# Performance work log

Measured on AMD Instinct MI355X. Metric: run time of the kernel, lower is better.

## Reference

```python
import jax, jax.numpy as jnp
import numpy as np

D_MODEL = 512
NUM_HEADS = 8
D_K = D_MODEL // NUM_HEADS
SCALE = D_K ** (-0.5)
B, L = 2, 256


def _tropical_linear(x, W, b):
    # max-plus linear: y[..., o] = max_i (x[..., i] + W[o, i]) + b[o]
    # x: (B, L, Din), W: (Dout, Din)
    return jnp.max(x[:, :, None, :] + W[None, None, :, :], axis=-1) + b


def _split_heads(t):
    Bn, Ln, Dn = t.shape
    return t.reshape(Bn, Ln, NUM_HEADS, D_K).transpose(0, 2, 1, 3)  # (B,H,L,dk)


def setup_inputs() -> dict:
    key = jax.random.key(0)
    ks = jax.random.split(key, 8)
    s = 1.0 / np.sqrt(D_MODEL)
    return {
        "x": jax.random.normal(ks[0], (B, L, D_MODEL), jnp.float32),
        "qW": jax.random.normal(ks[1], (D_MODEL, D_MODEL), jnp.float32) * s,
        "qb": jnp.zeros((D_MODEL,), jnp.float32),
        "kW": jax.random.normal(ks[2], (D_MODEL, D_MODEL), jnp.float32) * s,
        "kb": jnp.zeros((D_MODEL,), jnp.float32),
        "vW": jax.random.normal(ks[3], (D_MODEL, D_MODEL), jnp.float32) * s,
        "vb": jnp.zeros((D_MODEL,), jnp.float32),
        "oW": jax.random.normal(ks[4], (D_MODEL, D_MODEL), jnp.float32) * s,
        "ob": jnp.zeros((D_MODEL,), jnp.float32),
        "gW": jnp.zeros((NUM_HEADS, D_MODEL), jnp.float32),  # torch init: zeros
        "gb": jnp.full((NUM_HEADS,), 2.0, jnp.float32),      # torch init: +2.0
        "temp": jnp.ones((NUM_HEADS,), jnp.float32),
    }


def reference(x, qW, qb, kW, kb, vW, vb, oW, ob, gW, gb, temp):
    Bn, Ln, Dn = x.shape
    Q = _split_heads(_tropical_linear(x, qW, qb))  # (B,H,L,dk)
    K = _split_heads(_tropical_linear(x, kW, kb))
    V = _split_heads(x @ vW.T + vb)

    class_scores = jnp.einsum('bhqd,bhkd->bhqk', Q, K) * SCALE
    # tropical max-plus scores: max_d (Q[q,d] + K[k,d])
    trop_scores = jnp.max(Q[:, :, :, None, :] + K[:, :, None, :, :], axis=-1) * SCALE

    g = jax.nn.sigmoid(x @ gW.T + gb)            # (B,L,H)
    g = g.transpose(0, 2, 1)[..., None]          # (B,H,L,1)
    scores = g * trop_scores + (1.0 - g) * class_scores

    # Maslov temperature softmax: per-head learnable temperature
    attn = jax.nn.softmax(scores / temp[None, :, None, None], axis=-1)

    out = jnp.einsum('bhqk,bhkd->bhqd', attn, V)
    out = out.transpose(0, 2, 1, 3).reshape(Bn, Ln, Dn)
    return out @ oW.T + ob, attn
```

## Files before the change

kernel.cpp:

```cpp
#include <hip/hip_runtime.h>
#include <math.h>

#define DM    512
#define LSEQ  256
#define NB    2
#define NH    8
#define DK    64
#define SCALEF 0.125f

__global__ __launch_bounds__(256) void qkvg_kernel(
    const float* __restrict__ x,
    const float* __restrict__ qW, const float* __restrict__ qb,
    const float* __restrict__ kW, const float* __restrict__ kb,
    const float* __restrict__ vW, const float* __restrict__ vb,
    const float* __restrict__ gW, const float* __restrict__ gb,
    float* __restrict__ Qo, float* __restrict__ Ko,
    float* __restrict__ Vo, float* __restrict__ go)
{
    const int tid = threadIdx.x;
    const int op  = blockIdx.z;

    if (op == 3) {
        if (blockIdx.y != 0) return;
        const int row = blockIdx.x * 32 + (tid >> 3);
        const int h   = tid & 7;
        const float4* xr = (const float4*)(x  + row * DM);
        const float4* wr = (const float4*)(gW + h  * DM);
        float acc = 0.f;
        #pragma unroll 8
        for (int i = 0; i < DM / 4; ++i) {
            float4 a = xr[i], w = wr[i];
            acc = fmaf(a.x, w.x, acc);
            acc = fmaf(a.y, w.y, acc);
            acc = fmaf(a.z, w.z, acc);
            acc = fmaf(a.w, w.w, acc);
        }
        acc += gb[h];
        go[row * NH + h] = 1.f / (1.f + __expf(-acc));
        return;
    }

    const float* __restrict__ W;
    const float* __restrict__ bias;
    float* __restrict__ out;
    bool trop;
    if      (op == 0) { W = qW; bias = qb; out = Qo; trop = true;  }
    else if (op == 1) { W = kW; bias = kb; out = Ko; trop = true;  }
    else              { W = vW; bias = vb; out = Vo; trop = false; }

    __shared__ float Xs[32][68];
    __shared__ float Ws[32][68];

    const int row0 = blockIdx.x * 32;
    const int col0 = blockIdx.y * 32;
    const int ty = tid >> 4, tx = tid & 15;
    const int ra = ty;
    const int c4 = tx * 4;

    const float* xp0 = x + (row0 + ra) * DM + c4;
    const float* xp1 = xp0 + 16 * DM;
    const float* wp0 = W + (col0 + ra) * DM + c4;
    const float* wp1 = wp0 + 16 * DM;

    float4 xv0 = *(const float4*)xp0;
    float4 xv1 = *(const float4*)xp1;
    float4 wv0 = *(const float4*)wp0;
    float4 wv1 = *(const float4*)wp1;

    const float init = trop ? -INFINITY : 0.f;
    float a00 = init, a01 = init, a10 = init, a11 = init;

    for (int k0 = 0; k0 < DM; k0 += 64) {
        __syncthreads();
        *(float4*)&Xs[ra     ][c4] = xv0;
        *(float4*)&Xs[ra + 16][c4] = xv1;
        *(float4*)&Ws[ra     ][c4] = wv0;
        *(float4*)&Ws[ra + 16][c4] = wv1;
        __syncthreads();
        if (k0 + 64 < DM) {
            xv0 = *(const float4*)(xp0 + k0 + 64);
            xv1 = *(const float4*)(xp1 + k0 + 64);
            wv0 = *(const float4*)(wp0 + k0 + 64);
            wv1 = *(const float4*)(wp1 + k0 + 64);
        }
        if (trop) {
            #pragma unroll
            for (int kq = 0; kq < 16; ++kq) {
                float4 x0 = *(const float4*)&Xs[ty*2    ][kq*4];
                float4 x1 = *(const float4*)&Xs[ty*2 + 1][kq*4];
                float4 w0 = *(const float4*)&Ws[tx*2    ][kq*4];
                float4 w1 = *(const float4*)&Ws[tx*2 + 1][kq*4];
                a00 = fmaxf(fmaxf(a00, x0.x + w0.x), x0.y + w0.y);
                a00 = fmaxf(fmaxf(a00, x0.z + w0.z), x0.w + w0.w);
                a01 = fmaxf(fmaxf(a01, x0.x + w1.x), x0.y + w1.y);
                a01 = fmaxf(fmaxf(a01, x0.z + w1.z), x0.w + w1.w);
                a10 = fmaxf(fmaxf(a10, x1.x + w0.x), x1.y + w0.y);
                a10 = fmaxf(fmaxf(a10, x1.z + w0.z), x1.w + w0.w);
                a11 = fmaxf(fmaxf(a11, x1.x + w1.x), x1.y + w1.y);
                a11 = fmaxf(fmaxf(a11, x1.z + w1.z), x1.w + w1.w);
            }
        } else {
            #pragma unroll
            for (int kq = 0; kq < 16; ++kq) {
                float4 x0 = *(const float4*)&Xs[ty*2    ][kq*4];
                float4 x1 = *(const float4*)&Xs[ty*2 + 1][kq*4];
                float4 w0 = *(const float4*)&Ws[tx*2    ][kq*4];
                float4 w1 = *(const float4*)&Ws[tx*2 + 1][kq*4];
                a00 = fmaf(x0.x, w0.x, a00); a00 = fmaf(x0.y, w0.y, a00);
                a00 = fmaf(x0.z, w0.z, a00); a00 = fmaf(x0.w, w0.w, a00);
                a01 = fmaf(x0.x, w1.x, a01); a01 = fmaf(x0.y, w1.y, a01);
                a01 = fmaf(x0.z, w1.z, a01); a01 = fmaf(x0.w, w1.w, a01);
                a10 = fmaf(x1.x, w0.x, a10); a10 = fmaf(x1.y, w0.y, a10);
                a10 = fmaf(x1.z, w0.z, a10); a10 = fmaf(x1.w, w0.w, a10);
                a11 = fmaf(x1.x, w1.x, a11); a11 = fmaf(x1.y, w1.y, a11);
                a11 = fmaf(x1.z, w1.z, a11); a11 = fmaf(x1.w, w1.w, a11);
            }
        }
    }

    const int r0 = row0 + ty * 2, c0 = col0 + tx * 2;
    const float b0 = bias[c0], b1 = bias[c0 + 1];
    *(float2*)&out[(size_t)r0      * DM + c0] = make_float2(a00 + b0, a01 + b1);
    *(float2*)&out[(size_t)(r0+1)  * DM + c0] = make_float2(a10 + b0, a11 + b1);
}

__global__ __launch_bounds__(512) void attn_kernel(
    const float* __restrict__ Q, const float* __restrict__ K,
    const float* __restrict__ V, const float* __restrict__ g,
    const float* __restrict__ temp,
    float* __restrict__ attn_out, float* __restrict__ hout)
{
    const int tid = threadIdx.x;
    const int bh  = blockIdx.y;
    const int b   = bh >> 3, h = bh & 7;
    const int q0  = blockIdx.x * 16;
    const int ty  = tid >> 5;
    const int tx  = tid & 31;

    __shared__ float Qs[16][68];
    __shared__ float KVs[64][68];
    __shared__ float Ss[16][260];

    if (tid < 256) {
        const int r = tid >> 4, c = (tid & 15) * 4;
        float4 v = *(const float4*)&Q[(b * LSEQ + q0 + r) * DM + h * DK + c];
        *(float4*)&Qs[r][c] = v;
    }
    const float gq   = g[(b * LSEQ + q0 + ty) * NH + h];
    const float invt = SCALEF / temp[h];

    for (int kt = 0; kt < 4; ++kt) {
        __syncthreads();
        #pragma unroll
        for (int i = 0; i < 2; ++i) {
            const int f = tid + 512 * i;
            const int r = f >> 4, c = (f & 15) * 4;
            float4 v = *(const float4*)&K[(b * LSEQ + kt * 64 + r) * DM + h * DK + c];
            *(float4*)&KVs[r][c] = v;
        }
        __syncthreads();
        float d0 = 0.f, d1 = 0.f;
        float t0 = -INFINITY, t1 = -INFINITY;
        #pragma unroll
        for (int dq = 0; dq < 16; ++dq) {
            float4 q  = *(const float4*)&Qs[ty][dq * 4];
            float4 k0 = *(const float4*)&KVs[tx     ][dq * 4];
            float4 k1 = *(const float4*)&KVs[tx + 32][dq * 4];
            d0 = fmaf(q.x, k0.x, d0); d0 = fmaf(q.y, k0.y, d0);
            d0 = fmaf(q.z, k0.z, d0); d0 = fmaf(q.w, k0.w, d0);
            d1 = fmaf(q.x, k1.x, d1); d1 = fmaf(q.y, k1.y, d1);
            d1 = fmaf(q.z, k1.z, d1); d1 = fmaf(q.w, k1.w, d1);
            t0 = fmaxf(fmaxf(t0, q.x + k0.x), q.y + k0.y);
            t0 = fmaxf(fmaxf(t0, q.z + k0.z), q.w + k0.w);
            t1 = fmaxf(fmaxf(t1, q.x + k1.x), q.y + k1.y);
            t1 = fmaxf(fmaxf(t1, q.z + k1.z), q.w + k1.w);
        }
        Ss[ty][kt*64 + tx     ] = (gq * t0 + (1.f - gq) * d0) * invt;
        Ss[ty][kt*64 + tx + 32] = (gq * t1 + (1.f - gq) * d1) * invt;
    }
    __syncthreads();

    {
        float m = -INFINITY;
        #pragma unroll
        for (int j = 0; j < 8; ++j) m = fmaxf(m, Ss[ty][tx + 32 * j]);
        #pragma unroll
        for (int o = 16; o; o >>= 1) m = fmaxf(m, __shfl_xor(m, o));
        float s = 0.f;
        #pragma unroll
        for (int j = 0; j < 8; ++j) {
            const float e = __expf(Ss[ty][tx + 32 * j] - m);
            Ss[ty][tx + 32 * j] = e;
            s += e;
        }
        #pragma unroll
        for (int o = 16; o; o >>= 1) s += __shfl_xor(s, o);
        const float rs = 1.f / s;
        #pragma unroll
        for (int j = 0; j < 8; ++j) Ss[ty][tx + 32 * j] *= rs;
    }
    __syncthreads();

    {
        float* dst = attn_out + (size_t)(bh * LSEQ + q0) * LSEQ;
        #pragma unroll
        for (int i = 0; i < 2; ++i) {
            const int fi  = i * 2048 + tid * 4;
            const int row = fi >> 8, col = fi & 255;
            float4 v = *(const float4*)&Ss[row][col];
            *(float4*)&dst[fi] = v;
        }
    }

    float acc0 = 0.f, acc1 = 0.f;
    for (int kt = 0; kt < 4; ++kt) {
        __syncthreads();
        #pragma unroll
        for (int i = 0; i < 2; ++i) {
            const int f = tid + 512 * i;
            const int r = f >> 4, c = (f & 15) * 4;
            float4 v = *(const float4*)&V[(b * LSEQ + kt * 64 + r) * DM + h * DK + c];
            *(float4*)&KVs[r][c] = v;
        }
        __syncthreads();
        #pragma unroll
        for (int kq = 0; kq < 16; ++kq) {
            float4 a = *(const float4*)&Ss[ty][kt * 64 + kq * 4];
            const int k = kq * 4;
            float2 v0 = *(const float2*)&KVs[k    ][tx * 2];
            float2 v1 = *(const float2*)&KVs[k + 1][tx * 2];
            float2 v2 = *(const float2*)&KVs[k + 2][tx * 2];
            float2 v3 = *(const float2*)&KVs[k + 3][tx * 2];
            acc0 = fmaf(a.x, v0.x, acc0); acc1 = fmaf(a.x, v0.y, acc1);
            acc0 = fmaf(a.y, v1.x, acc0); acc1 = fmaf(a.y, v1.y, acc1);
            acc0 = fmaf(a.z, v2.x, acc0); acc1 = fmaf(a.z, v2.y, acc1);
            acc0 = fmaf(a.w, v3.x, acc0); acc1 = fmaf(a.w, v3.y, acc1);
        }
    }
    *(float2*)&hout[(size_t)(bh * LSEQ + q0 + ty) * DK + tx * 2] =
        make_float2(acc0, acc1);
}

__global__ __launch_bounds__(256) void oproj_kernel(
    const float* __restrict__ hout,
    const float* __restrict__ oW, const float* __restrict__ ob,
    float* __restrict__ out)
{
    __shared__ float Xs[32][68];
    __shared__ float Ws[32][68];
    const int tid = threadIdx.x;
    const int ty = tid >> 4, tx = tid & 15;
    const int row0 = blockIdx.x * 32;
    const int col0 = blockIdx.y * 32;
    const int ra = ty;
    const int c4 = tx * 4;

    const int grow = row0 + ra;
    const int bb = grow >> 8, ll = grow & 255;

    const float* wp0 = oW + (col0 + ra) * DM + c4;
    const float* wp1 = wp0 + 16 * DM;

    float a00 = 0.f, a01 = 0.f, a10 = 0.f, a11 = 0.f;

    float4 xv0 = *(const float4*)&hout[((bb * NH + 0) * LSEQ + ll     ) * DK + c4];
    float4 xv1 = *(const float4*)&hout[((bb * NH + 0) * LSEQ + ll + 16) * DK + c4];
    float4 wv0 = *(const float4*)wp0;
    float4 wv1 = *(const float4*)wp1;

    for (int k0 = 0; k0 < DM; k0 += 64) {
        __syncthreads();
        *(float4*)&Xs[ra     ][c4] = xv0;
        *(float4*)&Xs[ra + 16][c4] = xv1;
        *(float4*)&Ws[ra     ][c4] = wv0;
        *(float4*)&Ws[ra + 16][c4] = wv1;
        __syncthreads();
        if (k0 + 64 < DM) {
            const int hh = (k0 >> 6) + 1;
            xv0 = *(const float4*)&hout[((bb * NH + hh) * LSEQ + ll     ) * DK + c4];
            xv1 = *(const float4*)&hout[((bb * NH + hh) * LSEQ + ll + 16) * DK + c4];
            wv0 = *(const float4*)(wp0 + k0 + 64);
            wv1 = *(const float4*)(wp1 + k0 + 64);
        }
        #pragma unroll
        for (int kq = 0; kq < 16; ++kq) {
            float4 x0 = *(const float4*)&Xs[ty*2    ][kq*4];
            float4 x1 = *(const float4*)&Xs[ty*2 + 1][kq*4];
            float4 w0 = *(const float4*)&Ws[tx*2    ][kq*4];
            float4 w1 = *(const float4*)&Ws[tx*2 + 1][kq*4];
            a00 = fmaf(x0.x, w0.x, a00); a00 = fmaf(x0.y, w0.y, a00);
            a00 = fmaf(x0.z, w0.z, a00); a00 = fmaf(x0.w, w0.w, a00);
            a01 = fmaf(x0.x, w1.x, a01); a01 = fmaf(x0.y, w1.y, a01);
            a01 = fmaf(x0.z, w1.z, a01); a01 = fmaf(x0.w, w1.w, a01);
            a10 = fmaf(x1.x, w0.x, a10); a10 = fmaf(x1.y, w0.y, a10);
            a10 = fmaf(x1.z, w0.z, a10); a10 = fmaf(x1.w, w0.w, a10);
            a11 = fmaf(x1.x, w1.x, a11); a11 = fmaf(x1.y, w1.y, a11);
            a11 = fmaf(x1.z, w1.z, a11); a11 = fmaf(x1.w, w1.w, a11);
        }
    }

    const int r0 = row0 + ty * 2, c0 = col0 + tx * 2;
    const float b0 = ob[c0], b1 = ob[c0 + 1];
    *(float2*)&out[(size_t)r0     * DM + c0] = make_float2(a00 + b0, a01 + b1);
    *(float2*)&out[(size_t)(r0+1) * DM + c0] = make_float2(a10 + b0, a11 + b1);
}

extern "C" void kernel_launch(void* const* d_in, const int* in_sizes, int n_in,
                              void* d_out, int out_size, void* d_ws, size_t ws_size,
                              hipStream_t stream)
{
    const float* x    = (const float*)d_in[0];
    const float* qW   = (const float*)d_in[1];
    const float* qb   = (const float*)d_in[2];
    const float* kW   = (const float*)d_in[3];
    const float* kb   = (const float*)d_in[4];
    const float* vW   = (const float*)d_in[5];
    const float* vb   = (const float*)d_in[6];
    const float* oW   = (const float*)d_in[7];
    const float* ob   = (const float*)d_in[8];
    const float* gW   = (const float*)d_in[9];
    const float* gb   = (const float*)d_in[10];
    const float* temp = (const float*)d_in[11];

    float* out      = (float*)d_out;
    float* attn_out = out + NB * LSEQ * DM;

    float* ws   = (float*)d_ws;
    float* Qo   = ws;
    float* Ko   = Qo + NB * LSEQ * DM;
    float* Vo   = Ko + NB * LSEQ * DM;
    float* go   = Vo + NB * LSEQ * DM;
    float* hout = go + NB * LSEQ * NH;

    qkvg_kernel<<<dim3(16, 16, 4), 256, 0, stream>>>(
        x, qW, qb, kW, kb, vW, vb, gW, gb, Qo, Ko, Vo, go);
    attn_kernel<<<dim3(16, 16), 512, 0, stream>>>(
        Qo, Ko, Vo, go, temp, attn_out, hout);
    oproj_kernel<<<dim3(16, 16), 256, 0, stream>>>(
        hout, oW, ob, out);
}
```

Before: 163.8 us.

## Retile all three kernels with larger register tiles and transposed smem layouts

The QKV projection moves from 32x32 tiles with 2x2 outputs per thread to 64x64 tiles with 4x4 outputs per thread, using a k-major transposed shared layout and a flattened 1D grid of 192 GEMM blocks plus 16 gate blocks. The attention kernel drops to 256 threads, keeps Q in registers, stores K transposed, and computes 4 keys per thread. Head outputs are now written in (B,L,D) layout, so the output projection reads them contiguously using an outer-product 2x2 tile. The aim is more arithmetic per shared-memory load and less redundant traffic, at the cost of fewer blocks (lower occupancy and parallelism) and higher register pressure.

```diff
diff --git a/kernel.cpp b/kernel.cpp
--- a/kernel.cpp
+++ b/kernel.cpp
@@ -7,6 +7,7 @@
 #define NH    8
 #define DK    64
 #define SCALEF 0.125f
+#define KC    64
 
 __global__ __launch_bounds__(256) void qkvg_kernel(
     const float* __restrict__ x,
@@ -18,11 +19,11 @@
     float* __restrict__ Vo, float* __restrict__ go)
 {
     const int tid = threadIdx.x;
-    const int op  = blockIdx.z;
-
-    if (op == 3) {
-        if (blockIdx.y != 0) return;
-        const int row = blockIdx.x * 32 + (tid >> 3);
+    const int bx  = blockIdx.x;
+
+    if (bx >= 192) {
+        const int gx  = bx - 192;
+        const int row = gx * 32 + (tid >> 3);
         const int h   = tid & 7;
         const float4* xr = (const float4*)(x  + row * DM);
         const float4* wr = (const float4*)(gW + h  * DM);
@@ -40,6 +41,12 @@
         return;
     }
 
+    const int rt = bx / 24;
+    const int ct = bx % 24;
+    const int op = ct >> 3;
+    const int row0  = rt * 64;
+    const int col0m = (ct & 7) * 64;
+
     const float* __restrict__ W;
     const float* __restrict__ bias;
     float* __restrict__ out;
@@ -48,83 +55,101 @@
     else if (op == 1) { W = kW; bias = kb; out = Ko; trop = true;  }
     else              { W = vW; bias = vb; out = Vo; trop = false; }
 
-    __shared__ float Xs[32][68];
-    __shared__ float Ws[32][68];
-
-    const int row0 = blockIdx.x * 32;
-    const int col0 = blockIdx.y * 32;
+    __shared__ float Xs[KC][68];
+    __shared__ float Ws[KC][68];
+
     const int ty = tid >> 4, tx = tid & 15;
-    const int ra = ty;
-    const int c4 = tx * 4;
-
-    const float* xp0 = x + (row0 + ra) * DM + c4;
-    const float* xp1 = xp0 + 16 * DM;
-    const float* wp0 = W + (col0 + ra) * DM + c4;
-    const float* wp1 = wp0 + 16 * DM;
-
-    float4 xv0 = *(const float4*)xp0;
-    float4 xv1 = *(const float4*)xp1;
-    float4 wv0 = *(const float4*)wp0;
-    float4 wv1 = *(const float4*)wp1;
+    const int sr = tid & 63;
+    const int sq = tid >> 6;
+
+    const float* xp = x + (row0  + sr) * DM + sq * 16;
+    const float* wp = W + (col0m + sr) * DM + sq * 16;
+
+    float4 xg[4], wg[4];
+    #pragma unroll
+    for (int i = 0; i < 4; ++i) {
+        xg[i] = *(const float4*)(xp + i * 4);
+        wg[i] = *(const float4*)(wp + i * 4);
+    }
 
     const float init = trop ? -INFINITY : 0.f;
-    float a00 = init, a01 = init, a10 = init, a11 = init;
-
-    for (int k0 = 0; k0 < DM; k0 += 64) {
-        __syncthreads();
-        *(float4*)&Xs[ra     ][c4] = xv0;
-        *(float4*)&Xs[ra + 16][c4] = xv1;
-        *(float4*)&Ws[ra     ][c4] = wv0;
-        *(float4*)&Ws[ra + 16][c4] = wv1;
-        __syncthreads();
-        if (k0 + 64 < DM) {
-            xv0 = *(const float4*)(xp0 + k0 + 64);
-            xv1 = *(const float4*)(xp1 + k0 + 64);
-            wv0 = *(const float4*)(wp0 + k0 + 64);
-            wv1 = *(const float4*)(wp1 + k0 + 64);
+    float acc[4][4];
+    #pragma unroll
+    for (int i = 0; i < 4; ++i)
+        #pragma unroll
+        for (int j = 0; j < 4; ++j) acc[i][j] = init;
+
+    for (int k0 = 0; k0 < DM; k0 += KC) {
+        __syncthreads();
+        #pragma unroll
+        for (int i = 0; i < 4; ++i) {
+            const int kk = sq * 16 + i * 4;
+            Xs[kk + 0][sr] = xg[i].x;  Xs[kk + 1][sr] = xg[i].y;
+            Xs[kk + 2][sr] = xg[i].z;  Xs[kk + 3][sr] = xg[i].w;
+            Ws[kk + 0][sr] = wg[i].x;  Ws[kk + 1][sr] = wg[i].y;
+            Ws[kk + 2][sr] = wg[i].z;  Ws[kk + 3][sr] = wg[i].w;
+        }
+        __syncthreads();
+        if (k0 + KC < DM) {
+            #pragma unroll
+            for (int i = 0; i < 4; ++i) {
+                xg[i] = *(const float4*)(xp + k0 + KC + i * 4);
+                wg[i] = *(const float4*)(wp + k0 + KC + i * 4);
+            }
         }
         if (trop) {
-            #pragma unroll
-            for (int kq = 0; kq < 16; ++kq) {
-                float4 x0 = *(const float4*)&Xs[ty*2    ][kq*4];
-                float4 x1 = *(const float4*)&Xs[ty*2 + 1][kq*4];
-                float4 w0 = *(const float4*)&Ws[tx*2    ][kq*4];
-                float4 w1 = *(const float4*)&Ws[tx*2 + 1][kq*4];
-                a00 = fmaxf(fmaxf(a00, x0.x + w0.x), x0.y + w0.y);
-                a00 = fmaxf(fmaxf(a00, x0.z + w0.z), x0.w + w0.w);
-                a01 = fmaxf(fmaxf(a01, x0.x + w1.x), x0.y + w1.y);
-                a01 = fmaxf(fmaxf(a01, x0.z + w1.z), x0.w + w1.w);
-                a10 = fmaxf(fmaxf(a10, x1.x + w0.x), x1.y + w0.y);
-                a10 = fmaxf(fmaxf(a10, x1.z + w0.z), x1.w + w0.w);
-                a11 = fmaxf(fmaxf(a11, x1.x + w1.x), x1.y + w1.y);
-                a11 = fmaxf(fmaxf(a11, x1.z + w1.z), x1.w + w1.w);
+            #pragma unroll 4
+            for (int kp = 0; kp < KC / 2; ++kp) {
+                const int kk = kp * 2;
+                float4 x0 = *(const float4*)&Xs[kk    ][ty * 4];
+                float4 x1 = *(const float4*)&Xs[kk + 1][ty * 4];
+                float4 w0 = *(const float4*)&Ws[kk    ][tx * 4];
+                float4 w1 = *(const float4*)&Ws[kk + 1][tx * 4];
+                const float xa0[4] = {x0.x, x0.y, x0.z, x0.w};
+                const float xa1[4] = {x1.x, x1.y, x1.z, x1.w};
+                const float wa0[4] = {w0.x, w0.y, w0.z, w0.w};
+                const float wa1[4] = {w1.x, w1.y, w1.z, w1.w};
+                #pragma unroll
+                for (int i = 0; i < 4; ++i)
+                    #pragma unroll
+                    for (int j = 0; j < 4; ++j)
+                        acc[i][j] = fmaxf(fmaxf(acc[i][j], xa0[i] + wa0[j]),
+                                          xa1[i] + wa1[j]);
             }
         } else {
-            #pragma unroll
-            for (int kq = 0; kq < 16; ++kq) {
-                float4 x0 = *(const float4*)&Xs[ty*2    ][kq*4];
-                float4 x1 = *(const float4*)&Xs[ty*2 + 1][kq*4];
-                float4 w0 = *(const float4*)&Ws[tx*2    ][kq*4];
-                float4 w1 = *(const float4*)&Ws[tx*2 + 1][kq*4];
-                a00 = fmaf(x0.x, w0.x, a00); a00 = fmaf(x0.y, w0.y, a00);
-                a00 = fmaf(x0.z, w0.z, a00); a00 = fmaf(x0.w, w0.w, a00);
-                a01 = fmaf(x0.x, w1.x, a01); a01 = fmaf(x0.y, w1.y, a01);
-                a01 = fmaf(x0.z, w1.z, a01); a01 = fmaf(x0.w, w1.w, a01);
-                a10 = fmaf(x1.x, w0.x, a10); a10 = fmaf(x1.y, w0.y, a10);
-                a10 = fmaf(x1.z, w0.z, a10); a10 = fmaf(x1.w, w0.w, a10);
-                a11 = fmaf(x1.x, w1.x, a11); a11 = fmaf(x1.y, w1.y, a11);
-                a11 = fmaf(x1.z, w1.z, a11); a11 = fmaf(x1.w, w1.w, a11);
-            }
-        }
-    }
-
-    const int r0 = row0 + ty * 2, c0 = col0 + tx * 2;
-    const float b0 = bias[c0], b1 = bias[c0 + 1];
-    *(float2*)&out[(size_t)r0      * DM + c0] = make_float2(a00 + b0, a01 + b1);
-    *(float2*)&out[(size_t)(r0+1)  * DM + c0] = make_float2(a10 + b0, a11 + b1);
+            #pragma unroll 4
+            for (int kp = 0; kp < KC / 2; ++kp) {
+                const int kk = kp * 2;
+                float4 x0 = *(const float4*)&Xs[kk    ][ty * 4];
+                float4 x1 = *(const float4*)&Xs[kk + 1][ty * 4];
+                float4 w0 = *(const float4*)&Ws[kk    ][tx * 4];
+                float4 w1 = *(const float4*)&Ws[kk + 1][tx * 4];
+                const float xa0[4] = {x0.x, x0.y, x0.z, x0.w};
+                const float xa1[4] = {x1.x, x1.y, x1.z, x1.w};
+                const float wa0[4] = {w0.x, w0.y, w0.z, w0.w};
+                const float wa1[4] = {w1.x, w1.y, w1.z, w1.w};
+                #pragma unroll
+                for (int i = 0; i < 4; ++i)
+                    #pragma unroll
+                    for (int j = 0; j < 4; ++j) {
+                        acc[i][j] = fmaf(xa0[i], wa0[j], acc[i][j]);
+                        acc[i][j] = fmaf(xa1[i], wa1[j], acc[i][j]);
+                    }
+            }
+        }
+    }
+
+    const float4 bv = *(const float4*)&bias[col0m + tx * 4];
+    #pragma unroll
+    for (int i = 0; i < 4; ++i) {
+        const int r = row0 + ty * 4 + i;
+        float4 o = make_float4(acc[i][0] + bv.x, acc[i][1] + bv.y,
+                               acc[i][2] + bv.z, acc[i][3] + bv.w);
+        *(float4*)&out[(size_t)r * DM + col0m + tx * 4] = o;
+    }
 }
 
-__global__ __launch_bounds__(512) void attn_kernel(
+__global__ __launch_bounds__(256) void attn_kernel(
     const float* __restrict__ Q, const float* __restrict__ K,
     const float* __restrict__ V, const float* __restrict__ g,
     const float* __restrict__ temp,
@@ -134,111 +159,124 @@
     const int bh  = blockIdx.y;
     const int b   = bh >> 3, h = bh & 7;
     const int q0  = blockIdx.x * 16;
-    const int ty  = tid >> 5;
-    const int tx  = tid & 31;
-
-    __shared__ float Qs[16][68];
-    __shared__ float KVs[64][68];
+    const int ty  = tid >> 4, tx = tid & 15;
+
+    __shared__ float Kd[64][68];
+    __shared__ float Vs[64][68];
     __shared__ float Ss[16][260];
 
-    if (tid < 256) {
-        const int r = tid >> 4, c = (tid & 15) * 4;
-        float4 v = *(const float4*)&Q[(b * LSEQ + q0 + r) * DM + h * DK + c];
-        *(float4*)&Qs[r][c] = v;
-    }
+    const float* qrow = Q + (size_t)(b * LSEQ + q0 + ty) * DM + h * DK;
+    float4 qreg[16];
+    #pragma unroll
+    for (int i = 0; i < 16; ++i) qreg[i] = *(const float4*)(qrow + i * 4);
+
     const float gq   = g[(b * LSEQ + q0 + ty) * NH + h];
     const float invt = SCALEF / temp[h];
 
+    const int sr = tid & 63;
+    const int sq = tid >> 6;
+
     for (int kt = 0; kt < 4; ++kt) {
         __syncthreads();
-        #pragma unroll
-        for (int i = 0; i < 2; ++i) {
-            const int f = tid + 512 * i;
-            const int r = f >> 4, c = (f & 15) * 4;
-            float4 v = *(const float4*)&K[(b * LSEQ + kt * 64 + r) * DM + h * DK + c];
-            *(float4*)&KVs[r][c] = v;
-        }
-        __syncthreads();
-        float d0 = 0.f, d1 = 0.f;
-        float t0 = -INFINITY, t1 = -INFINITY;
-        #pragma unroll
-        for (int dq = 0; dq < 16; ++dq) {
-            float4 q  = *(const float4*)&Qs[ty][dq * 4];
-            float4 k0 = *(const float4*)&KVs[tx     ][dq * 4];
-            float4 k1 = *(const float4*)&KVs[tx + 32][dq * 4];
-            d0 = fmaf(q.x, k0.x, d0); d0 = fmaf(q.y, k0.y, d0);
-            d0 = fmaf(q.z, k0.z, d0); d0 = fmaf(q.w, k0.w, d0);
-            d1 = fmaf(q.x, k1.x, d1); d1 = fmaf(q.y, k1.y, d1);
-            d1 = fmaf(q.z, k1.z, d1); d1 = fmaf(q.w, k1.w, d1);
-            t0 = fmaxf(fmaxf(t0, q.x + k0.x), q.y + k0.y);
-            t0 = fmaxf(fmaxf(t0, q.z + k0.z), q.w + k0.w);
-            t1 = fmaxf(fmaxf(t1, q.x + k1.x), q.y + k1.y);
-            t1 = fmaxf(fmaxf(t1, q.z + k1.z), q.w + k1.w);
-        }
-        Ss[ty][kt*64 + tx     ] = (gq * t0 + (1.f - gq) * d0) * invt;
-        Ss[ty][kt*64 + tx + 32] = (gq * t1 + (1.f - gq) * d1) * invt;
+        {
+            const float* kp = K + (size_t)(b * LSEQ + kt * 64 + sr) * DM
+                              + h * DK + sq * 16;
+            #pragma unroll
+            for (int i = 0; i < 4; ++i) {
+                float4 v = *(const float4*)(kp + i * 4);
+                const int d = sq * 16 + i * 4;
+                Kd[d + 0][sr] = v.x;  Kd[d + 1][sr] = v.y;
+                Kd[d + 2][sr] = v.z;  Kd[d + 3][sr] = v.w;
+            }
+        }
+        __syncthreads();
+        float d0 = 0.f, d1 = 0.f, d2 = 0.f, d3 = 0.f;
+        float t0 = -INFINITY, t1 = -INFINITY, t2 = -INFINITY, t3 = -INFINITY;
+        #pragma unroll
+        for (int k4 = 0; k4 < 16; ++k4) {
+            const float4 q4 = qreg[k4];
+            float4 ka = *(const float4*)&Kd[k4 * 4 + 0][tx * 4];
+            float4 kb = *(const float4*)&Kd[k4 * 4 + 1][tx * 4];
+            float4 kc = *(const float4*)&Kd[k4 * 4 + 2][tx * 4];
+            float4 kd = *(const float4*)&Kd[k4 * 4 + 3][tx * 4];
+            d0 = fmaf(q4.x, ka.x, d0); d0 = fmaf(q4.y, kb.x, d0);
+            d0 = fmaf(q4.z, kc.x, d0); d0 = fmaf(q4.w, kd.x, d0);
+            d1 = fmaf(q4.x, ka.y, d1); d1 = fmaf(q4.y, kb.y, d1);
+            d1 = fmaf(q4.z, kc.y, d1); d1 = fmaf(q4.w, kd.y, d1);
+            d2 = fmaf(q4.x, ka.z, d2); d2 = fmaf(q4.y, kb.z, d2);
+            d2 = fmaf(q4.z, kc.z, d2); d2 = fmaf(q4.w, kd.z, d2);
+            d3 = fmaf(q4.x, ka.w, d3); d3 = fmaf(q4.y, kb.w, d3);
+            d3 = fmaf(q4.z, kc.w, d3); d3 = fmaf(q4.w, kd.w, d3);
+            t0 = fmaxf(fmaxf(t0, q4.x + ka.x), q4.y + kb.x);
+            t0 = fmaxf(fmaxf(t0, q4.z + kc.x), q4.w + kd.x);
+            t1 = fmaxf(fmaxf(t1, q4.x + ka.y), q4.y + kb.y);
+            t1 = fmaxf(fmaxf(t1, q4.z + kc.y), q4.w + kd.y);
+            t2 = fmaxf(fmaxf(t2, q4.x + ka.z), q4.y + kb.z);
+            t2 = fmaxf(fmaxf(t2, q4.z + kc.z), q4.w + kd.z);
+            t3 = fmaxf(fmaxf(t3, q4.x + ka.w), q4.y + kb.w);
+            t3 = fmaxf(fmaxf(t3, q4.z + kc.w), q4.w + kd.w);
+        }
+        const float gi = 1.f - gq;
+        *(float4*)&Ss[ty][kt * 64 + tx * 4] = make_float4(
+            (gq * t0 + gi * d0) * invt, (gq * t1 + gi * d1) * invt,
+            (gq * t2 + gi * d2) * invt, (gq * t3 + gi * d3) * invt);
     }
     __syncthreads();
 
     {
         float m = -INFINITY;
-        #pragma unroll
-        for (int j = 0; j < 8; ++j) m = fmaxf(m, Ss[ty][tx + 32 * j]);
-        #pragma unroll
-        for (int o = 16; o; o >>= 1) m = fmaxf(m, __shfl_xor(m, o));
+        #pragma unroll 4
+        for (int j = 0; j < 16; ++j) m = fmaxf(m, Ss[ty][tx + 16 * j]);
+        #pragma unroll
+        for (int o = 8; o; o >>= 1) m = fmaxf(m, __shfl_xor(m, o));
         float s = 0.f;
-        #pragma unroll
-        for (int j = 0; j < 8; ++j) {
-            const float e = __expf(Ss[ty][tx + 32 * j] - m);
-            Ss[ty][tx + 32 * j] = e;
+        #pragma unroll 4
+        for (int j = 0; j < 16; ++j) {
+            const float e = __expf(Ss[ty][tx + 16 * j] - m);
+            Ss[ty][tx + 16 * j] = e;
             s += e;
         }
         #pragma unroll
-        for (int o = 16; o; o >>= 1) s += __shfl_xor(s, o);
+        for (int o = 8; o; o >>= 1) s += __shfl_xor(s, o);
         const float rs = 1.f / s;
-        #pragma unroll
-        for (int j = 0; j < 8; ++j) Ss[ty][tx + 32 * j] *= rs;
-    }
-    __syncthreads();
+        #pragma unroll 4
+        for (int j = 0; j < 16; ++j) Ss[ty][tx + 16 * j] *= rs;
+    }
 
     {
-        float* dst = attn_out + (size_t)(bh * LSEQ + q0) * LSEQ;
-        #pragma unroll
-        for (int i = 0; i < 2; ++i) {
-            const int fi  = i * 2048 + tid * 4;
-            const int row = fi >> 8, col = fi & 255;
-            float4 v = *(const float4*)&Ss[row][col];
-            *(float4*)&dst[fi] = v;
-        }
-    }
-
-    float acc0 = 0.f, acc1 = 0.f;
+        float* dst = attn_out + (size_t)(bh * LSEQ + q0 + ty) * LSEQ;
+        #pragma unroll
+        for (int j = 0; j < 4; ++j)
+            *(float4*)&dst[j * 64 + tx * 4] =
+                *(const float4*)&Ss[ty][j * 64 + tx * 4];
+    }
+
+    float o0 = 0.f, o1 = 0.f, o2 = 0.f, o3 = 0.f;
+    const int vr = tid & 63;
+    const int vc = tid >> 6;
     for (int kt = 0; kt < 4; ++kt) {
         __syncthreads();
-        #pragma unroll
-        for (int i = 0; i < 2; ++i) {
-            const int f = tid + 512 * i;
-            const int r = f >> 4, c = (f & 15) * 4;
-            float4 v = *(const float4*)&V[(b * LSEQ + kt * 64 + r) * DM + h * DK + c];
-            *(float4*)&KVs[r][c] = v;
-        }
-        __syncthreads();
-        #pragma unroll
-        for (int kq = 0; kq < 16; ++kq) {
-            float4 a = *(const float4*)&Ss[ty][kt * 64 + kq * 4];
-            const int k = kq * 4;
-            float2 v0 = *(const float2*)&KVs[k    ][tx * 2];
-            float2 v1 = *(const float2*)&KVs[k + 1][tx * 2];
-            float2 v2 = *(const float2*)&KVs[k + 2][tx * 2];
-            float2 v3 = *(const float2*)&KVs[k + 3][tx * 2];
-            acc0 = fmaf(a.x, v0.x, acc0); acc1 = fmaf(a.x, v0.y, acc1);
-            acc0 = fmaf(a.y, v1.x, acc0); acc1 = fmaf(a.y, v1.y, acc1);
-            acc0 = fmaf(a.z, v2.x, acc0); acc1 = fmaf(a.z, v2.y, acc1);
-            acc0 = fmaf(a.w, v3.x, acc0); acc1 = fmaf(a.w, v3.y, acc1);
-        }
-    }
-    *(float2*)&hout[(size_t)(bh * LSEQ + q0 + ty) * DK + tx * 2] =
-        make_float2(acc0, acc1);
+        {
+            const float* vp = V + (size_t)(b * LSEQ + kt * 64 + vr) * DM
+                              + h * DK + vc * 16;
+            #pragma unroll
+            for (int i = 0; i < 4; ++i)
+                *(float4*)&Vs[vr][vc * 16 + i * 4] = *(const float4*)(vp + i * 4);
+        }
+        __syncthreads();
+        #pragma unroll 8
+        for (int k2 = 0; k2 < 32; ++k2) {
+            float2 a2 = *(const float2*)&Ss[ty][kt * 64 + k2 * 2];
+            float4 v0 = *(const float4*)&Vs[k2 * 2    ][tx * 4];
+            float4 v1 = *(const float4*)&Vs[k2 * 2 + 1][tx * 4];
+            o0 = fmaf(a2.x, v0.x, o0); o0 = fmaf(a2.y, v1.x, o0);
+            o1 = fmaf(a2.x, v0.y, o1); o1 = fmaf(a2.y, v1.y, o1);
+            o2 = fmaf(a2.x, v0.z, o2); o2 = fmaf(a2.y, v1.z, o2);
+            o3 = fmaf(a2.x, v0.w, o3); o3 = fmaf(a2.y, v1.w, o3);
+        }
+    }
+    *(float4*)&hout[(size_t)(b * LSEQ + q0 + ty) * DM + h * DK + tx * 4] =
+        make_float4(o0, o1, o2, o3);
 }
 
 __global__ __launch_bounds__(256) void oproj_kernel(
@@ -246,63 +284,63 @@
     const float* __restrict__ oW, const float* __restrict__ ob,
     float* __restrict__ out)
 {
-    __shared__ float Xs[32][68];
-    __shared__ float Ws[32][68];
     const int tid = threadIdx.x;
+    const int bx  = blockIdx.x;
+    const int row0 = (bx >> 4) * 32;
+    const int col0 = (bx & 15) * 32;
+
+    __shared__ float Xs[KC][36];
+    __shared__ float Ws[KC][36];
+
     const int ty = tid >> 4, tx = tid & 15;
-    const int row0 = blockIdx.x * 32;
-    const int col0 = blockIdx.y * 32;
-    const int ra = ty;
-    const int c4 = tx * 4;
-
-    const int grow = row0 + ra;
-    const int bb = grow >> 8, ll = grow & 255;
-
-    const float* wp0 = oW + (col0 + ra) * DM + c4;
-    const float* wp1 = wp0 + 16 * DM;
+    const int sr = tid & 31;
+    const int sq = tid >> 5;
+
+    const float* xp = hout + (size_t)(row0 + sr) * DM + sq * 8;
+    const float* wp = oW   + (size_t)(col0 + sr) * DM + sq * 8;
+
+    float4 xg[2], wg[2];
+    #pragma unroll
+    for (int i = 0; i < 2; ++i) {
+        xg[i] = *(const float4*)(xp + i * 4);
+        wg[i] = *(const float4*)(wp + i * 4);
+    }
 
     float a00 = 0.f, a01 = 0.f, a10 = 0.f, a11 = 0.f;
 
-    float4 xv0 = *(const float4*)&hout[((bb * NH + 0) * LSEQ + ll     ) * DK + c4];
-    float4 xv1 = *(const float4*)&hout[((bb * NH + 0) * LSEQ + ll + 16) * DK + c4];
-    float4 wv0 = *(const float4*)wp0;
-    float4 wv1 = *(const float4*)wp1;
-
-    for (int k0 = 0; k0 < DM; k0 += 64) {
-        __syncthreads();
-        *(float4*)&Xs[ra     ][c4] = xv0;
-        *(float4*)&Xs[ra + 16][c4] = xv1;
-        *(float4*)&Ws[ra     ][c4] = wv0;
-        *(float4*)&Ws[ra + 16][c4] = wv1;
-        __syncthreads();
-        if (k0 + 64 < DM) {
-            const int hh = (k0 >> 6) + 1;
-            xv0 = *(const float4*)&hout[((bb * NH + hh) * LSEQ + ll     ) * DK + c4];
-            xv1 = *(const float4*)&hout[((bb * NH + hh) * LSEQ + ll + 16) * DK + c4];
-            wv0 = *(const float4*)(wp0 + k0 + 64);
-            wv1 = *(const float4*)(wp1 + k0 + 64);
-        }
-        #pragma unroll
-        for (int kq = 0; kq < 16; ++kq) {
-            float4 x0 = *(const float4*)&Xs[ty*2    ][kq*4];
-            float4 x1 = *(const float4*)&Xs[ty*2 + 1][kq*4];
-            float4 w0 = *(const float4*)&Ws[tx*2    ][kq*4];
-            float4 w1 = *(const float4*)&Ws[tx*2 + 1][kq*4];
-            a00 = fmaf(x0.x, w0.x, a00); a00 = fmaf(x0.y, w0.y, a00);
-            a00 = fmaf(x0.z, w0.z, a00); a00 = fmaf(x0.w, w0.w, a00);
-            a01 = fmaf(x0.x, w1.x, a01); a01 = fmaf(x0.y, w1.y, a01);
-            a01 = fmaf(x0.z, w1.z, a01); a01 = fmaf(x0.w, w1.w, a01);
-            a10 = fmaf(x1.x, w0.x, a10); a10 = fmaf(x1.y, w0.y, a10);
-            a10 = fmaf(x1.z, w0.z, a10); a10 = fmaf(x1.w, w0.w, a10);
-            a11 = fmaf(x1.x, w1.x, a11); a11 = fmaf(x1.y, w1.y, a11);
-            a11 = fmaf(x1.z, w1.z, a11); a11 = fmaf(x1.w, w1.w, a11);
+    for (int k0 = 0; k0 < DM; k0 += KC) {
+        __syncthreads();
+        #pragma unroll
+        for (int i = 0; i < 2; ++i) {
+            const int kk = sq * 8 + i * 4;
+            Xs[kk + 0][sr] = xg[i].x;  Xs[kk + 1][sr] = xg[i].y;
+            Xs[kk + 2][sr] = xg[i].z;  Xs[kk + 3][sr] = xg[i].w;
+            Ws[kk + 0][sr] = wg[i].x;  Ws[kk + 1][sr] = wg[i].y;
+            Ws[kk + 2][sr] = wg[i].z;  Ws[kk + 3][sr] = wg[i].w;
+        }
+        __syncthreads();
+        if (k0 + KC < DM) {
+            #pragma unroll
+            for (int i = 0; i < 2; ++i) {
+                xg[i] = *(const float4*)(xp + k0 + KC + i * 4);
+                wg[i] = *(const float4*)(wp + k0 + KC + i * 4);
+            }
+        }
+        #pragma unroll 8
+        for (int kk = 0; kk < KC; ++kk) {
+            float2 xv = *(const float2*)&Xs[kk][ty * 2];
+            float2 wv = *(const float2*)&Ws[kk][tx * 2];
+            a00 = fmaf(xv.x, wv.x, a00);
+            a01 = fmaf(xv.x, wv.y, a01);
+            a10 = fmaf(xv.y, wv.x, a10);
+            a11 = fmaf(xv.y, wv.y, a11);
         }
     }
 
     const int r0 = row0 + ty * 2, c0 = col0 + tx * 2;
     const float b0 = ob[c0], b1 = ob[c0 + 1];
-    *(float2*)&out[(size_t)r0     * DM + c0] = make_float2(a00 + b0, a01 + b1);
-    *(float2*)&out[(size_t)(r0+1) * DM + c0] = make_float2(a10 + b0, a11 + b1);
+    *(float2*)&out[(size_t)r0       * DM + c0] = make_float2(a00 + b0, a01 + b1);
+    *(float2*)&out[(size_t)(r0 + 1) * DM + c0] = make_float2(a10 + b0, a11 + b1);
 }
 
 extern "C" void kernel_launch(void* const* d_in, const int* in_sizes, int n_in,
@@ -332,10 +370,10 @@
     float* go   = Vo + NB * LSEQ * DM;
     float* hout = go + NB * LSEQ * NH;
 
-    qkvg_kernel<<<dim3(16, 16, 4), 256, 0, stream>>>(
+    qkvg_kernel<<<dim3(208), 256, 0, stream>>>(
         x, qW, qb, kW, kb, vW, vb, gW, gb, Qo, Ko, Vo, go);
-    attn_kernel<<<dim3(16, 16), 512, 0, stream>>>(
+    attn_kernel<<<dim3(16, 16), 256, 0, stream>>>(
         Qo, Ko, Vo, go, temp, attn_out, hout);
-    oproj_kernel<<<dim3(16, 16), 256, 0, stream>>>(
+    oproj_kernel<<<dim3(256), 256, 0, stream>>>(
         hout, oW, ob, out);
 }
```

Result: faster. 154.0 us (-6.0%).
